# Performance work log

Hardware: AMD Instinct MI355X
Metric: run time of the kernel (lower is better)

Reference implementation:

```python
import jax, jax.numpy as jnp
import numpy as np

N, IN_F, OUT_F = 8192, 4096, 4096
QMIN, QMAX = -128, 127  # int8 range for bitwidth 8


def setup_inputs() -> dict:
    key = jax.random.key(0)
    k1, k2, k3, k4 = jax.random.split(key, 4)
    x = jax.random.randint(k1, (N, IN_F), QMIN, QMAX + 1, dtype=jnp.int32).astype(jnp.int8)
    weight = jax.random.randint(k2, (OUT_F, IN_F), QMIN, QMAX + 1, dtype=jnp.int32).astype(jnp.int8)
    bias = jax.random.randint(k3, (OUT_F,), -1024, 1024, dtype=jnp.int32)
    weight_scale = jax.random.uniform(k4, (OUT_F,), dtype=jnp.float32, minval=0.001, maxval=0.02)
    input_scale = jnp.asarray([0.05], dtype=jnp.float32)
    output_scale = jnp.asarray([0.1], dtype=jnp.float32)
    output_zero_point = 0
    return {"x": x, "weight": weight, "bias": bias, "weight_scale": weight_scale,
            "input_scale": input_scale, "output_scale": output_scale,
            "output_zero_point": output_zero_point}


def reference(x, weight, bias, weight_scale, input_scale, output_scale, output_zero_point):
    # int32-accumulated GEMM with bias (CPU path of the torch module)
    acc = jnp.matmul(x.astype(jnp.int32), weight.astype(jnp.int32).T) + bias[None, :]  # [N, OUT_F] int32
    # fused dequant/requant epilogue
    scale_factor = (input_scale * weight_scale / output_scale)[None, :]  # [1, OUT_F]
    out = acc.astype(jnp.float32) * scale_factor + output_zero_point
    out = jnp.clip(jnp.round(out), QMIN, QMAX).astype(jnp.int8)
    return out
```

## Files before the change

kernel.cpp:

```cpp
#include <hip/hip_runtime.h>
#include <stdint.h>


#define M_DIM 8192
#define N_DIM 4096
#define K_DIM 4096
#define BM 256
#define BN 256
#define BKB 64
#define NKT (K_DIM / BKB)
#define NT NKT
#define NBLK ((M_DIM / BM) * (N_DIM / BN))
#define ABUF (BM * BKB)
#define BBUF (BN * BKB)

using i32x4 = __attribute__((ext_vector_type(4))) int;

typedef const __attribute__((address_space(1))) uint32_t* gptr_t;
typedef __attribute__((address_space(3))) uint32_t* lptr_t;

__device__ __forceinline__ void gload_lds16(const void* g, void* l) {
    __builtin_amdgcn_global_load_lds((gptr_t)g, (lptr_t)l, 16, 0, 0);
}

__device__ __forceinline__ int pack4(i32x4 v) {
    return (int)(((unsigned)v.x & 0xFFu) | (((unsigned)v.y & 0xFFu) << 8) |
                 (((unsigned)v.z & 0xFFu) << 16) | (((unsigned)v.w) << 24));
}

__global__ void pack_panels_kernel(const int* __restrict__ src, int8_t* __restrict__ dst,
                                   int n_blocks) {
    int gid = blockIdx.x * blockDim.x + threadIdx.x;
    int blk = gid >> 6;
    int l = gid & 63;
    if (blk >= n_blocks) return;
    int rb = blk >> 6;
    int kt = blk & (NKT - 1);
    const i32x4* s4 = (const i32x4*)(src + (size_t)(rb * 16 + (l & 15)) * K_DIM
                                         + kt * 64 + (l >> 4) * 16);
    i32x4 o;
    o.x = pack4(s4[0]); o.y = pack4(s4[1]); o.z = pack4(s4[2]); o.w = pack4(s4[3]);
    *(i32x4*)(dst + (size_t)blk * 1024 + l * 16) = o;
}

#define MFMA_I8(a, b, c) __builtin_amdgcn_mfma_i32_16x16x64_i8((a), (b), (c), 0, 0, 0)

#define FRAG_A(P, m) (*(const i32x4*)(Acur + ((P) * 4 + (m)) * 1024))
#define FRAG_B(n)    (*(const i32x4*)(Bcur + (n) * 1024))

#define PHASE0(STAGE_STMTS, TAIL_STMTS)                                           \
  { i32x4 af0 = FRAG_A(0,0), af1 = FRAG_A(0,1), af2 = FRAG_A(0,2), af3 = FRAG_A(0,3); \
    bq0 = FRAG_B(0); bq1 = FRAG_B(1); bq2 = FRAG_B(2); bq3 = FRAG_B(3);           \
    STAGE_STMTS;                                                                  \
    __builtin_amdgcn_s_barrier();                                                 \
    asm volatile("s_waitcnt lgkmcnt(0)" ::: "memory");                            \
    __builtin_amdgcn_sched_barrier(0);                                            \
    __builtin_amdgcn_s_setprio(1);                                                \
    acc[0][0]=MFMA_I8(af0,bq0,acc[0][0]); acc[0][1]=MFMA_I8(af0,bq1,acc[0][1]);   \
    acc[0][2]=MFMA_I8(af0,bq2,acc[0][2]); acc[0][3]=MFMA_I8(af0,bq3,acc[0][3]);   \
    acc[1][0]=MFMA_I8(af1,bq0,acc[1][0]); acc[1][1]=MFMA_I8(af1,bq1,acc[1][1]);   \
    acc[1][2]=MFMA_I8(af1,bq2,acc[1][2]); acc[1][3]=MFMA_I8(af1,bq3,acc[1][3]);   \
    acc[2][0]=MFMA_I8(af2,bq0,acc[2][0]); acc[2][1]=MFMA_I8(af2,bq1,acc[2][1]);   \
    acc[2][2]=MFMA_I8(af2,bq2,acc[2][2]); acc[2][3]=MFMA_I8(af2,bq3,acc[2][3]);   \
    acc[3][0]=MFMA_I8(af3,bq0,acc[3][0]); acc[3][1]=MFMA_I8(af3,bq1,acc[3][1]);   \
    acc[3][2]=MFMA_I8(af3,bq2,acc[3][2]); acc[3][3]=MFMA_I8(af3,bq3,acc[3][3]);   \
    __builtin_amdgcn_s_setprio(0);                                                \
    TAIL_STMTS;                                                                   \
    __builtin_amdgcn_s_barrier(); }

#define PHASE1(STAGE_STMTS, TAIL_STMTS)                                           \
  { i32x4 af0 = FRAG_A(1,0), af1 = FRAG_A(1,1), af2 = FRAG_A(1,2), af3 = FRAG_A(1,3); \
    STAGE_STMTS;                                                                  \
    __builtin_amdgcn_s_barrier();                                                 \
    asm volatile("s_waitcnt lgkmcnt(0)" ::: "memory");                            \
    __builtin_amdgcn_sched_barrier(0);                                            \
    __builtin_amdgcn_s_setprio(1);                                                \
    acc[4][0]=MFMA_I8(af0,bq0,acc[4][0]); acc[4][1]=MFMA_I8(af0,bq1,acc[4][1]);   \
    acc[4][2]=MFMA_I8(af0,bq2,acc[4][2]); acc[4][3]=MFMA_I8(af0,bq3,acc[4][3]);   \
    acc[5][0]=MFMA_I8(af1,bq0,acc[5][0]); acc[5][1]=MFMA_I8(af1,bq1,acc[5][1]);   \
    acc[5][2]=MFMA_I8(af1,bq2,acc[5][2]); acc[5][3]=MFMA_I8(af1,bq3,acc[5][3]);   \
    acc[6][0]=MFMA_I8(af2,bq0,acc[6][0]); acc[6][1]=MFMA_I8(af2,bq1,acc[6][1]);   \
    acc[6][2]=MFMA_I8(af2,bq2,acc[6][2]); acc[6][3]=MFMA_I8(af2,bq3,acc[6][3]);   \
    acc[7][0]=MFMA_I8(af3,bq0,acc[7][0]); acc[7][1]=MFMA_I8(af3,bq1,acc[7][1]);   \
    acc[7][2]=MFMA_I8(af3,bq2,acc[7][2]); acc[7][3]=MFMA_I8(af3,bq3,acc[7][3]);   \
    __builtin_amdgcn_s_setprio(0);                                                \
    TAIL_STMTS;                                                                   \
    __builtin_amdgcn_s_barrier(); }

__global__ __launch_bounds__(512, 2)
void qgemm256_kernel(const int8_t* __restrict__ xp, const int8_t* __restrict__ wp,
                     const int* __restrict__ bias, const float* __restrict__ wscale,
                     const float* __restrict__ iscale, const float* __restrict__ oscale,
                     const int* __restrict__ zp, int* __restrict__ out) {
    extern __shared__ int8_t lds[];
    int8_t* As = lds;
    int8_t* Bs = lds + 3 * ABUF;

    const int tid  = threadIdx.x;
    const int wave = tid >> 6;
    const int lane = tid & 63;

    int b = blockIdx.x;
    int s = (b & 7) * (NBLK >> 3) + (b >> 3);
    const int bcol = (s & 15) * BN;
    const int brow = (s >> 4) * BM;

    const int wr = wave >> 2;
    const int wc = wave & 3;

    const int rb0 = brow >> 4;
    const int cb0 = bcol >> 4;
    const int8_t* AgP = xp + ((size_t)(rb0 + wave * 2) * NKT) * 1024 + lane * 16;
    const int8_t* BgP = wp + ((size_t)(cb0 + wave * 2) * NKT) * 1024 + lane * 16;
    const size_t substep = (size_t)NKT * 1024;
    const int aoff = wave * 2048;

    i32x4 acc[8][4] = {};
    i32x4 bq0, bq1, bq2, bq3;

    #pragma unroll
    for (int t0 = 0; t0 < 2; t0++) {
        int8_t* Ad = As + t0 * ABUF;
        int8_t* Bd = Bs + t0 * BBUF;
        gload_lds16(AgP + (size_t)t0 * 1024,           Ad + aoff);
        gload_lds16(AgP + substep + (size_t)t0 * 1024, Ad + aoff + 1024);
        gload_lds16(BgP + (size_t)t0 * 1024,           Bd + aoff);
        gload_lds16(BgP + substep + (size_t)t0 * 1024, Bd + aoff + 1024);
    }
    asm volatile("s_waitcnt vmcnt(4)" ::: "memory");
    __builtin_amdgcn_s_barrier();

    int cur = 0, stg = 2;
    for (int t = 0; t < NT - 2; ++t) {
        const int8_t* Acur = As + cur * ABUF + wr * 8192 + lane * 16;
        const int8_t* Bcur = Bs + cur * BBUF + wc * 4096 + lane * 16;
        int8_t* Astg = As + stg * ABUF;
        int8_t* Bstg = Bs + stg * BBUF;
        const size_t koff = (size_t)(t + 2) * 1024;

        PHASE0(
            { gload_lds16(AgP + koff,           Astg + aoff);
              gload_lds16(AgP + substep + koff, Astg + aoff + 1024); },
            ((void)0))
        PHASE1(
            { gload_lds16(BgP + koff,           Bstg + aoff);
              gload_lds16(BgP + substep + koff, Bstg + aoff + 1024); },
            asm volatile("s_waitcnt vmcnt(4)" ::: "memory"))

        cur = (cur == 2) ? 0 : cur + 1;
        stg = (stg == 2) ? 0 : stg + 1;
    }
    {
        const int8_t* Acur = As + cur * ABUF + wr * 8192 + lane * 16;
        const int8_t* Bcur = Bs + cur * BBUF + wc * 4096 + lane * 16;
        PHASE0(((void)0), ((void)0))
        PHASE1(((void)0), asm volatile("s_waitcnt vmcnt(0)" ::: "memory"))
        cur = (cur == 2) ? 0 : cur + 1;
    }
    {
        const int8_t* Acur = As + cur * ABUF + wr * 8192 + lane * 16;
        const int8_t* Bcur = Bs + cur * BBUF + wc * 4096 + lane * 16;
        PHASE0(((void)0), ((void)0))
        PHASE1(((void)0), ((void)0))
    }

    const float is_v = iscale[0];
    const float os_v = oscale[0];
    const float zpf = (float)zp[0];
    #pragma unroll
    for (int n = 0; n < 4; n++) {
        int col = bcol + wc * 64 + n * 16 + (lane & 15);
        float sf = (is_v * wscale[col]) / os_v;
        int bz = bias[col];
        #pragma unroll
        for (int m = 0; m < 8; m++) {
            int row0 = brow + wr * 128 + m * 16 + (lane >> 4) * 4;
            #pragma unroll
            for (int r = 0; r < 4; r++) {
                float v = (float)(acc[m][n][r] + bz) * sf + zpf;
                v = rintf(v);
                v = fminf(fmaxf(v, -128.0f), 127.0f);
                out[(size_t)(row0 + r) * N_DIM + col] = (int)v;
            }
        }
    }
}

__global__ void qgemm_fallback(const int* __restrict__ x32, const int* __restrict__ w32,
                               const int* __restrict__ bias, const float* __restrict__ wscale,
                               const float* __restrict__ iscale, const float* __restrict__ oscale,
                               const int* __restrict__ zp, int* __restrict__ out) {
    __shared__ int8_t As[128][64];
    __shared__ int8_t Bs[128][64];
    const int tid  = threadIdx.x;
    const int wave = tid >> 6;
    const int lane = tid & 63;
    int b = blockIdx.x;
    int s = (b & 7) * (gridDim.x >> 3) + (b >> 3);
    const int bcol = (s & 31) * 128;
    const int brow = (s >> 5) * 128;
    const int wr = wave >> 1;
    const int wc = wave & 1;
    i32x4 acc[4][4] = {};
    for (int kt = 0; kt < K_DIM; kt += 64) {
        int row = tid >> 1;
        int h = tid & 1;
        const i32x4* sa = (const i32x4*)(x32 + (size_t)(brow + row) * K_DIM + kt + h * 32);
        const i32x4* sb = (const i32x4*)(w32 + (size_t)(bcol + row) * K_DIM + kt + h * 32);
        int pa[8], pb[8];
        #pragma unroll
        for (int j = 0; j < 8; j++) { pa[j] = pack4(sa[j]); pb[j] = pack4(sb[j]); }
        *(i32x4*)&As[row][h * 32]      = *(i32x4*)&pa[0];
        *(i32x4*)&As[row][h * 32 + 16] = *(i32x4*)&pa[4];
        *(i32x4*)&Bs[row][h * 32]      = *(i32x4*)&pb[0];
        *(i32x4*)&Bs[row][h * 32 + 16] = *(i32x4*)&pb[4];
        __syncthreads();
        i32x4 a_frag[4], b_frag[4];
        #pragma unroll
        for (int m = 0; m < 4; m++)
            a_frag[m] = *(const i32x4*)&As[wr * 64 + m * 16 + (lane & 15)][(lane >> 4) * 16];
        #pragma unroll
        for (int n = 0; n < 4; n++)
            b_frag[n] = *(const i32x4*)&Bs[wc * 64 + n * 16 + (lane & 15)][(lane >> 4) * 16];
        #pragma unroll
        for (int m = 0; m < 4; m++)
            #pragma unroll
            for (int n = 0; n < 4; n++)
                acc[m][n] = MFMA_I8(a_frag[m], b_frag[n], acc[m][n]);
        __syncthreads();
    }
    const float is_v = iscale[0];
    const float os_v = oscale[0];
    const float zpf = (float)zp[0];
    #pragma unroll
    for (int n = 0; n < 4; n++) {
        int col = bcol + wc * 64 + n * 16 + (lane & 15);
        float sf = (is_v * wscale[col]) / os_v;
        int bz = bias[col];
        #pragma unroll
        for (int m = 0; m < 4; m++) {
            int row0 = brow + wr * 64 + m * 16 + (lane >> 4) * 4;
            #pragma unroll
            for (int r = 0; r < 4; r++) {
                float v = (float)(acc[m][n][r] + bz) * sf + zpf;
                v = rintf(v);
                v = fminf(fmaxf(v, -128.0f), 127.0f);
                out[(size_t)(row0 + r) * N_DIM + col] = (int)v;
            }
        }
    }
}

extern "C" void kernel_launch(void* const* d_in, const int* in_sizes, int n_in,
                              void* d_out, int out_size, void* d_ws, size_t ws_size,
                              hipStream_t stream) {
    const int*   x32    = (const int*)d_in[0];
    const int*   w32    = (const int*)d_in[1];
    const int*   bias   = (const int*)d_in[2];
    const float* wscale = (const float*)d_in[3];
    const float* iscale = (const float*)d_in[4];
    const float* oscale = (const float*)d_in[5];
    const int*   zp     = (const int*)d_in[6];
    int* out = (int*)d_out;

    const size_t need = (size_t)M_DIM * K_DIM + (size_t)N_DIM * K_DIM;
    const size_t lds_bytes = 3 * (size_t)(ABUF + BBUF);

    if (ws_size >= need) {
        int8_t* xp = (int8_t*)d_ws;
        int8_t* wp = xp + (size_t)M_DIM * K_DIM;
        const int nblkA = (M_DIM / 16) * NKT;
        const int nblkB = (N_DIM / 16) * NKT;
        pack_panels_kernel<<<nblkA / 4, 256, 0, stream>>>(x32, xp, nblkA);
        pack_panels_kernel<<<nblkB / 4, 256, 0, stream>>>(w32, wp, nblkB);
        (void)hipFuncSetAttribute((const void*)qgemm256_kernel,
                                  hipFuncAttributeMaxDynamicSharedMemorySize,
                                  (int)lds_bytes);
        qgemm256_kernel<<<NBLK, 512, lds_bytes, stream>>>(xp, wp, bias, wscale, iscale, oscale, zp, out);
    } else {
        qgemm_fallback<<<2048, 256, 0, stream>>>(x32, w32, bias, wscale, iscale, oscale, zp, out);
    }
}
```

Baseline: 187.6 us.

## Switch int8 GEMM to 32x32x32 MFMA with matching 32-row panel packing

Replaces the 16x16x64 int8 MFMA tiling with 32x32x32 MFMA instructions. The pack kernel now builds 32-row by 32-k panels, and each wave computes a 4x2 grid of 32x32 accumulators instead of 8x4 16x16 tiles. Each K step issues fewer, larger MFMAs and needs fewer LDS fragment reads per unit of math, which is meant to raise matrix-core utilisation. The epilogue is remapped to the 32x32 accumulator layout, which changes the output store pattern.

```diff
diff --git a/kernel.cpp b/kernel.cpp
--- a/kernel.cpp
+++ b/kernel.cpp
@@ -7,14 +7,14 @@
 #define K_DIM 4096
 #define BM 256
 #define BN 256
-#define BKB 64
-#define NKT (K_DIM / BKB)
-#define NT NKT
+#define NKT2 (K_DIM / 32)
+#define NT (K_DIM / 64)
 #define NBLK ((M_DIM / BM) * (N_DIM / BN))
-#define ABUF (BM * BKB)
-#define BBUF (BN * BKB)
-
-using i32x4 = __attribute__((ext_vector_type(4))) int;
+#define ABUF (BM * 64)
+#define BBUF (BN * 64)
+
+using i32x4  = __attribute__((ext_vector_type(4))) int;
+using i32x16 = __attribute__((ext_vector_type(16))) int;
 
 typedef const __attribute__((address_space(1))) uint32_t* gptr_t;
 typedef __attribute__((address_space(3))) uint32_t* lptr_t;
@@ -28,70 +28,47 @@
                  (((unsigned)v.z & 0xFFu) << 16) | (((unsigned)v.w) << 24));
 }
 
-__global__ void pack_panels_kernel(const int* __restrict__ src, int8_t* __restrict__ dst,
-                                   int n_blocks) {
+__global__ void pack_panels32_kernel(const int* __restrict__ src, int8_t* __restrict__ dst,
+                                     int n_blocks) {
     int gid = blockIdx.x * blockDim.x + threadIdx.x;
     int blk = gid >> 6;
     int l = gid & 63;
     if (blk >= n_blocks) return;
-    int rb = blk >> 6;
-    int kt = blk & (NKT - 1);
-    const i32x4* s4 = (const i32x4*)(src + (size_t)(rb * 16 + (l & 15)) * K_DIM
-                                         + kt * 64 + (l >> 4) * 16);
+    int rb = blk >> 7;
+    int kt = blk & (NKT2 - 1);
+    const i32x4* s4 = (const i32x4*)(src + (size_t)(rb * 32 + (l & 31)) * K_DIM
+                                         + kt * 32 + (l >> 5) * 16);
     i32x4 o;
     o.x = pack4(s4[0]); o.y = pack4(s4[1]); o.z = pack4(s4[2]); o.w = pack4(s4[3]);
     *(i32x4*)(dst + (size_t)blk * 1024 + l * 16) = o;
 }
 
-#define MFMA_I8(a, b, c) __builtin_amdgcn_mfma_i32_16x16x64_i8((a), (b), (c), 0, 0, 0)
-
-#define FRAG_A(P, m) (*(const i32x4*)(Acur + ((P) * 4 + (m)) * 1024))
-#define FRAG_B(n)    (*(const i32x4*)(Bcur + (n) * 1024))
-
-#define PHASE0(STAGE_STMTS, TAIL_STMTS)                                           \
-  { i32x4 af0 = FRAG_A(0,0), af1 = FRAG_A(0,1), af2 = FRAG_A(0,2), af3 = FRAG_A(0,3); \
-    bq0 = FRAG_B(0); bq1 = FRAG_B(1); bq2 = FRAG_B(2); bq3 = FRAG_B(3);           \
+#define MFMA32(a, b, c) __builtin_amdgcn_mfma_i32_32x32x32_i8((a), (b), (c), 0, 0, 0)
+
+#define FRAG_A(r, k) (*(const i32x4*)(Acur + (r) * 2048 + (k) * 1024))
+#define FRAG_B(c, k) (*(const i32x4*)(Bcur + (c) * 2048 + (k) * 1024))
+
+#define PHASEK(k, STAGE_STMTS, TAIL_STMTS)                                        \
+  { i32x4 a0 = FRAG_A(0,k), a1 = FRAG_A(1,k), a2 = FRAG_A(2,k), a3 = FRAG_A(3,k); \
+    i32x4 b0 = FRAG_B(0,k), b1 = FRAG_B(1,k);                                     \
     STAGE_STMTS;                                                                  \
     __builtin_amdgcn_s_barrier();                                                 \
     asm volatile("s_waitcnt lgkmcnt(0)" ::: "memory");                            \
     __builtin_amdgcn_sched_barrier(0);                                            \
     __builtin_amdgcn_s_setprio(1);                                                \
-    acc[0][0]=MFMA_I8(af0,bq0,acc[0][0]); acc[0][1]=MFMA_I8(af0,bq1,acc[0][1]);   \
-    acc[0][2]=MFMA_I8(af0,bq2,acc[0][2]); acc[0][3]=MFMA_I8(af0,bq3,acc[0][3]);   \
-    acc[1][0]=MFMA_I8(af1,bq0,acc[1][0]); acc[1][1]=MFMA_I8(af1,bq1,acc[1][1]);   \
-    acc[1][2]=MFMA_I8(af1,bq2,acc[1][2]); acc[1][3]=MFMA_I8(af1,bq3,acc[1][3]);   \
-    acc[2][0]=MFMA_I8(af2,bq0,acc[2][0]); acc[2][1]=MFMA_I8(af2,bq1,acc[2][1]);   \
-    acc[2][2]=MFMA_I8(af2,bq2,acc[2][2]); acc[2][3]=MFMA_I8(af2,bq3,acc[2][3]);   \
-    acc[3][0]=MFMA_I8(af3,bq0,acc[3][0]); acc[3][1]=MFMA_I8(af3,bq1,acc[3][1]);   \
-    acc[3][2]=MFMA_I8(af3,bq2,acc[3][2]); acc[3][3]=MFMA_I8(af3,bq3,acc[3][3]);   \
+    acc[0][0] = MFMA32(a0, b0, acc[0][0]); acc[0][1] = MFMA32(a0, b1, acc[0][1]); \
+    acc[1][0] = MFMA32(a1, b0, acc[1][0]); acc[1][1] = MFMA32(a1, b1, acc[1][1]); \
+    acc[2][0] = MFMA32(a2, b0, acc[2][0]); acc[2][1] = MFMA32(a2, b1, acc[2][1]); \
+    acc[3][0] = MFMA32(a3, b0, acc[3][0]); acc[3][1] = MFMA32(a3, b1, acc[3][1]); \
     __builtin_amdgcn_s_setprio(0);                                                \
     TAIL_STMTS;                                                                   \
     __builtin_amdgcn_s_barrier(); }
 
-#define PHASE1(STAGE_STMTS, TAIL_STMTS)                                           \
-  { i32x4 af0 = FRAG_A(1,0), af1 = FRAG_A(1,1), af2 = FRAG_A(1,2), af3 = FRAG_A(1,3); \
-    STAGE_STMTS;                                                                  \
-    __builtin_amdgcn_s_barrier();                                                 \
-    asm volatile("s_waitcnt lgkmcnt(0)" ::: "memory");                            \
-    __builtin_amdgcn_sched_barrier(0);                                            \
-    __builtin_amdgcn_s_setprio(1);                                                \
-    acc[4][0]=MFMA_I8(af0,bq0,acc[4][0]); acc[4][1]=MFMA_I8(af0,bq1,acc[4][1]);   \
-    acc[4][2]=MFMA_I8(af0,bq2,acc[4][2]); acc[4][3]=MFMA_I8(af0,bq3,acc[4][3]);   \
-    acc[5][0]=MFMA_I8(af1,bq0,acc[5][0]); acc[5][1]=MFMA_I8(af1,bq1,acc[5][1]);   \
-    acc[5][2]=MFMA_I8(af1,bq2,acc[5][2]); acc[5][3]=MFMA_I8(af1,bq3,acc[5][3]);   \
-    acc[6][0]=MFMA_I8(af2,bq0,acc[6][0]); acc[6][1]=MFMA_I8(af2,bq1,acc[6][1]);   \
-    acc[6][2]=MFMA_I8(af2,bq2,acc[6][2]); acc[6][3]=MFMA_I8(af2,bq3,acc[6][3]);   \
-    acc[7][0]=MFMA_I8(af3,bq0,acc[7][0]); acc[7][1]=MFMA_I8(af3,bq1,acc[7][1]);   \
-    acc[7][2]=MFMA_I8(af3,bq2,acc[7][2]); acc[7][3]=MFMA_I8(af3,bq3,acc[7][3]);   \
-    __builtin_amdgcn_s_setprio(0);                                                \
-    TAIL_STMTS;                                                                   \
-    __builtin_amdgcn_s_barrier(); }
-
 __global__ __launch_bounds__(512, 2)
-void qgemm256_kernel(const int8_t* __restrict__ xp, const int8_t* __restrict__ wp,
-                     const int* __restrict__ bias, const float* __restrict__ wscale,
-                     const float* __restrict__ iscale, const float* __restrict__ oscale,
-                     const int* __restrict__ zp, int* __restrict__ out) {
+void qgemm32_kernel(const int8_t* __restrict__ xp, const int8_t* __restrict__ wp,
+                    const int* __restrict__ bias, const float* __restrict__ wscale,
+                    const float* __restrict__ iscale, const float* __restrict__ oscale,
+                    const int* __restrict__ zp, int* __restrict__ out) {
     extern __shared__ int8_t lds[];
     int8_t* As = lds;
     int8_t* Bs = lds + 3 * ABUF;
@@ -108,24 +85,22 @@
     const int wr = wave >> 2;
     const int wc = wave & 3;
 
-    const int rb0 = brow >> 4;
-    const int cb0 = bcol >> 4;
-    const int8_t* AgP = xp + ((size_t)(rb0 + wave * 2) * NKT) * 1024 + lane * 16;
-    const int8_t* BgP = wp + ((size_t)(cb0 + wave * 2) * NKT) * 1024 + lane * 16;
-    const size_t substep = (size_t)NKT * 1024;
+    const int rb0 = brow >> 5;
+    const int cb0 = bcol >> 5;
+    const int8_t* AgP = xp + ((size_t)(rb0 + wave) * NKT2) * 1024 + lane * 16;
+    const int8_t* BgP = wp + ((size_t)(cb0 + wave) * NKT2) * 1024 + lane * 16;
     const int aoff = wave * 2048;
 
-    i32x4 acc[8][4] = {};
-    i32x4 bq0, bq1, bq2, bq3;
+    i32x16 acc[4][2] = {};
 
     #pragma unroll
     for (int t0 = 0; t0 < 2; t0++) {
         int8_t* Ad = As + t0 * ABUF;
         int8_t* Bd = Bs + t0 * BBUF;
-        gload_lds16(AgP + (size_t)t0 * 1024,           Ad + aoff);
-        gload_lds16(AgP + substep + (size_t)t0 * 1024, Ad + aoff + 1024);
-        gload_lds16(BgP + (size_t)t0 * 1024,           Bd + aoff);
-        gload_lds16(BgP + substep + (size_t)t0 * 1024, Bd + aoff + 1024);
+        gload_lds16(AgP + (size_t)(2 * t0) * 1024,     Ad + aoff);
+        gload_lds16(AgP + (size_t)(2 * t0 + 1) * 1024, Ad + aoff + 1024);
+        gload_lds16(BgP + (size_t)(2 * t0) * 1024,     Bd + aoff);
+        gload_lds16(BgP + (size_t)(2 * t0 + 1) * 1024, Bd + aoff + 1024);
     }
     asm volatile("s_waitcnt vmcnt(4)" ::: "memory");
     __builtin_amdgcn_s_barrier();
@@ -136,15 +111,15 @@
         const int8_t* Bcur = Bs + cur * BBUF + wc * 4096 + lane * 16;
         int8_t* Astg = As + stg * ABUF;
         int8_t* Bstg = Bs + stg * BBUF;
-        const size_t koff = (size_t)(t + 2) * 1024;
-
-        PHASE0(
-            { gload_lds16(AgP + koff,           Astg + aoff);
-              gload_lds16(AgP + substep + koff, Astg + aoff + 1024); },
+        const size_t k0 = (size_t)(2 * (t + 2)) * 1024;
+
+        PHASEK(0,
+            { gload_lds16(AgP + k0,        Astg + aoff);
+              gload_lds16(AgP + k0 + 1024, Astg + aoff + 1024); },
             ((void)0))
-        PHASE1(
-            { gload_lds16(BgP + koff,           Bstg + aoff);
-              gload_lds16(BgP + substep + koff, Bstg + aoff + 1024); },
+        PHASEK(1,
+            { gload_lds16(BgP + k0,        Bstg + aoff);
+              gload_lds16(BgP + k0 + 1024, Bstg + aoff + 1024); },
             asm volatile("s_waitcnt vmcnt(4)" ::: "memory"))
 
         cur = (cur == 2) ? 0 : cur + 1;
@@ -153,38 +128,41 @@
     {
         const int8_t* Acur = As + cur * ABUF + wr * 8192 + lane * 16;
         const int8_t* Bcur = Bs + cur * BBUF + wc * 4096 + lane * 16;
-        PHASE0(((void)0), ((void)0))
-        PHASE1(((void)0), asm volatile("s_waitcnt vmcnt(0)" ::: "memory"))
+        PHASEK(0, ((void)0), ((void)0))
+        PHASEK(1, ((void)0), asm volatile("s_waitcnt vmcnt(0)" ::: "memory"))
         cur = (cur == 2) ? 0 : cur + 1;
     }
     {
         const int8_t* Acur = As + cur * ABUF + wr * 8192 + lane * 16;
         const int8_t* Bcur = Bs + cur * BBUF + wc * 4096 + lane * 16;
-        PHASE0(((void)0), ((void)0))
-        PHASE1(((void)0), ((void)0))
+        PHASEK(0, ((void)0), ((void)0))
+        PHASEK(1, ((void)0), ((void)0))
     }
 
     const float is_v = iscale[0];
     const float os_v = oscale[0];
     const float zpf = (float)zp[0];
     #pragma unroll
-    for (int n = 0; n < 4; n++) {
-        int col = bcol + wc * 64 + n * 16 + (lane & 15);
+    for (int c = 0; c < 2; c++) {
+        int col = bcol + wc * 64 + c * 32 + (lane & 31);
         float sf = (is_v * wscale[col]) / os_v;
         int bz = bias[col];
         #pragma unroll
-        for (int m = 0; m < 8; m++) {
-            int row0 = brow + wr * 128 + m * 16 + (lane >> 4) * 4;
+        for (int r = 0; r < 4; r++) {
+            int rowb = brow + wr * 128 + r * 32 + 4 * (lane >> 5);
             #pragma unroll
-            for (int r = 0; r < 4; r++) {
-                float v = (float)(acc[m][n][r] + bz) * sf + zpf;
+            for (int reg = 0; reg < 16; reg++) {
+                int row = rowb + (reg & 3) + 8 * (reg >> 2);
+                float v = (float)(acc[r][c][reg] + bz) * sf + zpf;
                 v = rintf(v);
                 v = fminf(fmaxf(v, -128.0f), 127.0f);
-                out[(size_t)(row0 + r) * N_DIM + col] = (int)v;
+                out[(size_t)row * N_DIM + col] = (int)v;
             }
         }
     }
 }
+
+#define MFMA_I8(a, b, c) __builtin_amdgcn_mfma_i32_16x16x64_i8((a), (b), (c), 0, 0, 0)
 
 __global__ void qgemm_fallback(const int* __restrict__ x32, const int* __restrict__ w32,
                                const int* __restrict__ bias, const float* __restrict__ wscale,
@@ -269,14 +247,14 @@
     if (ws_size >= need) {
         int8_t* xp = (int8_t*)d_ws;
         int8_t* wp = xp + (size_t)M_DIM * K_DIM;
-        const int nblkA = (M_DIM / 16) * NKT;
-        const int nblkB = (N_DIM / 16) * NKT;
-        pack_panels_kernel<<<nblkA / 4, 256, 0, stream>>>(x32, xp, nblkA);
-        pack_panels_kernel<<<nblkB / 4, 256, 0, stream>>>(w32, wp, nblkB);
-        (void)hipFuncSetAttribute((const void*)qgemm256_kernel,
+        const int nblkA = (M_DIM / 32) * NKT2;
+        const int nblkB = (N_DIM / 32) * NKT2;
+        pack_panels32_kernel<<<nblkA / 4, 256, 0, stream>>>(x32, xp, nblkA);
+        pack_panels32_kernel<<<nblkB / 4, 256, 0, stream>>>(w32, wp, nblkB);
+        (void)hipFuncSetAttribute((const void*)qgemm32_kernel,
                                   hipFuncAttributeMaxDynamicSharedMemorySize,
                                   (int)lds_bytes);
-        qgemm256_kernel<<<NBLK, 512, lds_bytes, stream>>>(xp, wp, bias, wscale, iscale, oscale, zp, out);
+        qgemm32_kernel<<<NBLK, 512, lds_bytes, stream>>>(xp, wp, bias, wscale, iscale, oscale, zp, out);
     } else {
         qgemm_fallback<<<2048, 256, 0, stream>>>(x32, w32, bias, wscale, iscale, oscale, zp, out);
     }
```

New measurement: 187.2 us. No clear change (-0.2%).
